# Kernel tuning notes

Hardware: AMD Instinct MI355X
Metric: run time of the kernel (lower is better)

The kernel has to match this reference:

```python
import jax, jax.numpy as jnp
import numpy as np

L = 2       # num_layers
D = 256     # d_model
DFF = 1024  # d_ffn
NH = 8      # n_heads
NP = 4      # n_points
CIN = 512   # in_channels
B = 8
HH = 64
WW = 64
EPS = 1e-5


def setup_inputs() -> dict:
    key = jax.random.key(0)
    ks = iter(jax.random.split(key, 48))
    def w(shape, s=0.02):
        return jax.random.normal(next(ks), shape, jnp.float32) * s
    inp = dict(
        x=jax.random.normal(next(ks), (B, CIN, HH, WW), jnp.float32),
        W_in=w((D, CIN)),
        bn1_g=jnp.ones((D,), jnp.float32), bn1_b=jnp.zeros((D,), jnp.float32),
        bn1_m=jnp.zeros((D,), jnp.float32), bn1_v=jnp.ones((D,), jnp.float32),
        query_embed=w((HH * WW, D), 1.0),
        Woff=w((L, D, NH * NP * 2)), boff=w((L, NH * NP * 2), 2.0),
        Wattn=w((L, D, NH * NP)), battn=jnp.zeros((L, NH * NP), jnp.float32),
        Wval=w((L, D, D)), bval=jnp.zeros((L, D), jnp.float32),
        Wo=w((L, D, D)), bo=jnp.zeros((L, D), jnp.float32),
        ln1_g=jnp.ones((L, D), jnp.float32), ln1_b=jnp.zeros((L, D), jnp.float32),
        W1=w((L, D, DFF)), b1=jnp.zeros((L, DFF), jnp.float32),
        W2=w((L, DFF, D)), b2=jnp.zeros((L, D), jnp.float32),
        ln2_g=jnp.ones((L, D), jnp.float32), ln2_b=jnp.zeros((L, D), jnp.float32),
        W_out=w((CIN, D)),
        bn2_g=jnp.ones((CIN,), jnp.float32), bn2_b=jnp.zeros((CIN,), jnp.float32),
        bn2_m=jnp.zeros((CIN,), jnp.float32), bn2_v=jnp.ones((CIN,), jnp.float32),
    )
    return inp


def layer_norm(x, g, b):
    m = jnp.mean(x, axis=-1, keepdims=True)
    v = jnp.mean((x - m) ** 2, axis=-1, keepdims=True)
    return (x - m) * jax.lax.rsqrt(v + EPS) * g + b


def bilinear_sample(value, loc, Hh, Ww):
    # value: (B, NH, dh, H*W); loc: (B, Lq, NH, NP, 2) normalized to [0,1]
    # Matches F.grid_sample(align_corners=False, padding_mode='zeros') with grid=2*loc-1.
    Bn, Lq, nH, P, _ = loc.shape
    gx = loc[..., 0] * Ww - 0.5
    gy = loc[..., 1] * Hh - 0.5
    x0 = jnp.floor(gx)
    y0 = jnp.floor(gy)
    wx = gx - x0
    wy = gy - y0
    x0i = x0.astype(jnp.int32)
    y0i = y0.astype(jnp.int32)

    def t(a):  # (B,Lq,NH,P) -> (B,NH,1,Lq*P)
        return jnp.transpose(a, (0, 2, 1, 3)).reshape(Bn, nH, 1, Lq * P)

    def gather(xi, yi):
        valid = (xi >= 0) & (xi < Ww) & (yi >= 0) & (yi < Hh)
        xc = jnp.clip(xi, 0, Ww - 1)
        yc = jnp.clip(yi, 0, Hh - 1)
        idx = t(yc * Ww + xc)  # (B,NH,1,Lq*P)
        v = jnp.take_along_axis(value, idx, axis=3)  # (B,NH,dh,Lq*P)
        return v * t(valid).astype(value.dtype)

    v00 = gather(x0i, y0i)
    v10 = gather(x0i + 1, y0i)
    v01 = gather(x0i, y0i + 1)
    v11 = gather(x0i + 1, y0i + 1)
    wxt = t(wx)
    wyt = t(wy)
    out = (v00 * (1 - wxt) * (1 - wyt) + v10 * wxt * (1 - wyt)
           + v01 * (1 - wxt) * wyt + v11 * wxt * wyt)
    return out.reshape(Bn, nH, -1, Lq, P)  # (B,NH,dh,Lq,NP)


def reference(x, W_in, bn1_g, bn1_b, bn1_m, bn1_v, query_embed,
              Woff, boff, Wattn, battn, Wval, bval, Wo, bo,
              ln1_g, ln1_b, W1, b1, W2, b2, ln2_g, ln2_b,
              W_out, bn2_g, bn2_b, bn2_m, bn2_v):
    Bn, C, Hh, Ww = x.shape
    HW = Hh * Ww
    dh = D // NH

    # proj_in: 1x1 conv (no bias) + BN (inference) + ReLU
    xp = jnp.einsum('bchw,dc->bdhw', x, W_in)
    xp = (xp - bn1_m[:, None, None]) * jax.lax.rsqrt(bn1_v[:, None, None] + EPS)
    xp = jax.nn.relu(xp * bn1_g[:, None, None] + bn1_b[:, None, None])
    src = xp.reshape(Bn, D, HW).transpose(0, 2, 1)  # (B, HW, D)

    # reference points: centers of pixels, normalized
    ry = (jnp.arange(Hh, dtype=jnp.float32) + 0.5) / Hh
    rx = (jnp.arange(Ww, dtype=jnp.float32) + 0.5) / Ww
    yy, xx = jnp.meshgrid(ry, rx, indexing='ij')
    refpts = jnp.stack([xx, yy], axis=-1).reshape(HW, 2)  # (HW, 2) as (x, y)
    norm = jnp.array([Ww, Hh], jnp.float32)

    q = jnp.broadcast_to(query_embed[None], (Bn, HW, D))
    for i in range(L):
        # --- MSDeformAttn (n_levels=1) ---
        val = (src @ Wval[i] + bval[i]).reshape(Bn, HW, NH, dh)
        val = val.transpose(0, 2, 3, 1)  # (B, NH, dh, HW)
        off = (q @ Woff[i] + boff[i]).reshape(Bn, HW, NH, NP, 2)
        attn = jax.nn.softmax((q @ Wattn[i] + battn[i]).reshape(Bn, HW, NH, NP), axis=-1)
        loc = refpts[None, :, None, None, :] + off / norm  # (B, HW, NH, NP, 2)
        samp = bilinear_sample(val, loc, Hh, Ww)  # (B, NH, dh, HW, NP)
        o = jnp.einsum('bhdqp,bhqp->bqhd', samp, attn.transpose(0, 2, 1, 3))
        o = o.reshape(Bn, HW, D) @ Wo[i] + bo[i]
        q = layer_norm(q + o, ln1_g[i], ln1_b[i])
        # --- FFN ---
        ffn = jax.nn.relu(q @ W1[i] + b1[i]) @ W2[i] + b2[i]
        q = layer_norm(q + ffn, ln2_g[i], ln2_b[i])

    # proj_out: 1x1 conv (no bias) + BN (inference) + ReLU
    y = q.transpose(0, 2, 1).reshape(Bn, D, Hh, Ww)
    y = jnp.einsum('bdhw,cd->bchw', y, W_out)
    y = (y - bn2_m[:, None, None]) * jax.lax.rsqrt(bn2_v[:, None, None] + EPS)
    return jax.nn.relu(y * bn2_g[:, None, None] + bn2_b[:, None, None])
```

## Files before the change

### kernel.cpp

```cpp
#include <hip/hip_runtime.h>
#include <cstdint>

#define LYR 2
#define DM  256
#define DFFN 1024
#define CINC 512
#define BBATCH 8
#define HWTOT 4096
#define EPSV 1e-5f

using u16 = unsigned short;
typedef __attribute__((ext_vector_type(8))) short bf16x8;
typedef __attribute__((ext_vector_type(4))) float f32x4;

__device__ inline u16 f2b(float v) {
    union { float f; uint32_t u; } x; x.f = v;
    uint32_t r = x.u + 0x7fffu + ((x.u >> 16) & 1u);
    return (u16)(r >> 16);
}
__device__ inline uint32_t pk2(float a, float b) {
    return (uint32_t)f2b(a) | ((uint32_t)f2b(b) << 16);
}
__device__ inline float blo(uint32_t d) {
    union { uint32_t i; float f; } x; x.i = d << 16; return x.f;
}
__device__ inline float bhi(uint32_t d) {
    union { uint32_t i; float f; } x; x.i = d & 0xffff0000u; return x.f;
}

template<int MODE>
__global__ __launch_bounds__(256) void mfma_gemm(
    const u16* __restrict__ A, const u16* __restrict__ Bt,
    const float* __restrict__ scale, const float* __restrict__ shift,
    void* __restrict__ Cv, int M, int N, int K, int ldc,
    long long a_zs, long long b_zs, long long c_zs, int swz, int gxlog)
{
    __shared__ u16 As[4][4096];
    __shared__ u16 Bs[4][4096];
    const int tid = threadIdx.x;
    const int lane = tid & 63;
    const int wid = tid >> 6;
    const int wm = (wid & 1) << 6, wn = (wid >> 1) << 6;
    const int quad = lane >> 4, r = lane & 15;

    int bx = blockIdx.x, by = blockIdx.y;
    if (swz) {
        int linear = by * gridDim.x + bx;
        int xcd = linear & 7;
        int s = linear >> 3;
        bx = s & (gridDim.x - 1);
        by = xcd * (gridDim.y >> 3) + (s >> gxlog);
    }
    const int m0 = by << 7, n0 = bx << 7;
    const u16* Ab = A + (long long)blockIdx.z * a_zs + (long long)m0 * K;
    const u16* Bb = Bt + (long long)blockIdx.z * b_zs + (long long)n0 * K;

    const int u0 = tid, u1 = tid + 256;
    const int mu0 = u0 >> 2, cu0 = (u0 & 3) ^ ((mu0 >> 1) & 3);
    const int mu1 = u1 >> 2, cu1 = (u1 & 3) ^ ((mu1 >> 1) & 3);
    const long long ga0 = (long long)mu0 * K + cu0 * 8;
    const long long ga1 = (long long)mu1 * K + cu1 * 8;

    int aoff[4], boff[4];
#pragma unroll
    for (int t = 0; t < 4; ++t) {
        int m = wm + t * 16 + r;
        aoff[t] = (m * 4 + (quad ^ ((m >> 1) & 3))) * 8;
        int n = wn + t * 16 + r;
        boff[t] = (n * 4 + (quad ^ ((n >> 1) & 3))) * 8;
    }

    f32x4 acc[4][4];
#pragma unroll
    for (int i = 0; i < 4; ++i)
#pragma unroll
        for (int j = 0; j < 4; ++j) acc[i][j] = (f32x4){0.f, 0.f, 0.f, 0.f};

    const int NT = K >> 5;

#define GSTAGE(g, b) do {                                                                       \
    const long long kk = (long long)(g) << 5;                                                   \
    __builtin_amdgcn_global_load_lds((const __attribute__((address_space(1))) void*)(Ab + ga0 + kk), \
        (__attribute__((address_space(3))) void*)(&As[b][u0 * 8]), 16, 0, 0);                   \
    __builtin_amdgcn_global_load_lds((const __attribute__((address_space(1))) void*)(Ab + ga1 + kk), \
        (__attribute__((address_space(3))) void*)(&As[b][u1 * 8]), 16, 0, 0);                   \
    __builtin_amdgcn_global_load_lds((const __attribute__((address_space(1))) void*)(Bb + ga0 + kk), \
        (__attribute__((address_space(3))) void*)(&Bs[b][u0 * 8]), 16, 0, 0);                   \
    __builtin_amdgcn_global_load_lds((const __attribute__((address_space(1))) void*)(Bb + ga1 + kk), \
        (__attribute__((address_space(3))) void*)(&Bs[b][u1 * 8]), 16, 0, 0);                   \
} while (0)

    GSTAGE(0, 0);
    GSTAGE(1, 1);
    GSTAGE(2, 2);

    for (int t = 0; t < NT; ++t) {
        if (t < NT - 2)       asm volatile("s_waitcnt vmcnt(8)" ::: "memory");
        else if (t == NT - 2) asm volatile("s_waitcnt vmcnt(4)" ::: "memory");
        else                  asm volatile("s_waitcnt vmcnt(0)" ::: "memory");
        __builtin_amdgcn_s_barrier();
        __builtin_amdgcn_sched_barrier(0);
        if (t + 3 < NT) GSTAGE(t + 3, (t + 3) & 3);
        const u16* Ap = As[t & 3];
        const u16* Bp = Bs[t & 3];
        bf16x8 af[4], bf[4];
#pragma unroll
        for (int tt = 0; tt < 4; ++tt) af[tt] = *(const bf16x8*)(Ap + aoff[tt]);
#pragma unroll
        for (int tt = 0; tt < 4; ++tt) bf[tt] = *(const bf16x8*)(Bp + boff[tt]);
#pragma unroll
        for (int i = 0; i < 4; ++i)
#pragma unroll
            for (int j = 0; j < 4; ++j)
                acc[i][j] = __builtin_amdgcn_mfma_f32_16x16x32_bf16(bf[j], af[i], acc[i][j], 0, 0, 0);
    }
#undef GSTAGE

    const long long zc = (long long)blockIdx.z * c_zs;
    float4 sh4[4], sc4[4];
    if (MODE != 3) {
#pragma unroll
        for (int j = 0; j < 4; ++j) {
            int colb = n0 + wn + j * 16 + quad * 4;
            sh4[j] = *(const float4*)&shift[colb];
            if (MODE == 1) sc4[j] = *(const float4*)&scale[colb];
        }
    }
#pragma unroll
    for (int i = 0; i < 4; ++i) {
        const int row = m0 + wm + i * 16 + r;
        float rsc = 0.f, rsh = 0.f;
        if (MODE == 3) { rsc = scale[row]; rsh = shift[row]; }
#pragma unroll
        for (int j = 0; j < 4; ++j) {
            const int colb = n0 + wn + j * 16 + quad * 4;
            f32x4 v = acc[i][j];
            if (MODE == 0) {
                uint2 o;
                o.x = pk2(v[0] + sh4[j].x, v[1] + sh4[j].y);
                o.y = pk2(v[2] + sh4[j].z, v[3] + sh4[j].w);
                *(uint2*)((u16*)Cv + zc + (long long)row * ldc + colb) = o;
            } else if (MODE == 1) {
                uint2 o;
                o.x = pk2(fmaxf(v[0] * sc4[j].x + sh4[j].x, 0.f), fmaxf(v[1] * sc4[j].y + sh4[j].y, 0.f));
                o.y = pk2(fmaxf(v[2] * sc4[j].z + sh4[j].z, 0.f), fmaxf(v[3] * sc4[j].w + sh4[j].w, 0.f));
                *(uint2*)((u16*)Cv + zc + (long long)row * ldc + colb) = o;
            } else if (MODE == 2) {
                float4 o = {v[0] + sh4[j].x, v[1] + sh4[j].y, v[2] + sh4[j].z, v[3] + sh4[j].w};
                *(float4*)((float*)Cv + zc + (long long)row * ldc + colb) = o;
            } else {
                float4 o = {fmaxf(v[0] * rsc + rsh, 0.f), fmaxf(v[1] * rsc + rsh, 0.f),
                            fmaxf(v[2] * rsc + rsh, 0.f), fmaxf(v[3] * rsc + rsh, 0.f)};
                *(float4*)((float*)Cv + zc + (long long)row * ldc + colb) = o;
            }
        }
    }
}

__global__ __launch_bounds__(512, 4) void mfma_gemm_ln(
    const u16* __restrict__ A, const u16* __restrict__ Bf,
    const float* __restrict__ bias,
    float* __restrict__ q, u16* __restrict__ q16,
    const float* __restrict__ g, const float* __restrict__ beta, int K)
{
    __shared__ u16 As[3][2048];
    __shared__ float red_s[8][64], red_ss[8][64];
    const int tid = threadIdx.x;
    const int lane = tid & 63;
    const int w = tid >> 6;
    const int quad = lane >> 4, r = lane & 15;
    const int m0 = blockIdx.x << 6;
    const u16* Ab = A + (long long)m0 * K;

    const int mA = tid >> 2, cA = (tid & 3) ^ ((mA >> 1) & 3);
    const long long gaA = (long long)mA * K + cA * 8;
    const bool stager = tid < 256;

    int aoff[4];
#pragma unroll
    for (int t = 0; t < 4; ++t) {
        int m = t * 16 + r;
        aoff[t] = (m * 4 + (quad ^ ((m >> 1) & 3))) * 8;
    }

    const u16* Bw = Bf + ((size_t)(2 * w) * 64 + lane) * 8;

    f32x4 acc[4][2];
#pragma unroll
    for (int i = 0; i < 4; ++i)
#pragma unroll
        for (int j = 0; j < 2; ++j) acc[i][j] = (f32x4){0.f, 0.f, 0.f, 0.f};

    const int NT = K >> 5;

    if (stager) {
        __builtin_amdgcn_global_load_lds((const __attribute__((address_space(1))) void*)(Ab + gaA),
                                         (__attribute__((address_space(3))) void*)(&As[0][tid * 8]), 16, 0, 0);
        __builtin_amdgcn_global_load_lds((const __attribute__((address_space(1))) void*)(Ab + gaA + 32),
                                         (__attribute__((address_space(3))) void*)(&As[1][tid * 8]), 16, 0, 0);
    }
    __builtin_amdgcn_sched_barrier(0);
    bf16x8 bc0 = *(const bf16x8*)(Bw);
    bf16x8 bc1 = *(const bf16x8*)(Bw + 512);

    int cb = 0;
    for (int t = 0; t < NT; ++t) {
        asm volatile("s_waitcnt vmcnt(3)" ::: "memory");
        __builtin_amdgcn_s_barrier();
        __builtin_amdgcn_sched_barrier(0);
        int nb = cb + 2; if (nb >= 3) nb -= 3;
        if (stager && t + 2 < NT)
            __builtin_amdgcn_global_load_lds((const __attribute__((address_space(1))) void*)(Ab + gaA + (long long)(t + 2) * 32),
                                             (__attribute__((address_space(3))) void*)(&As[nb][tid * 8]), 16, 0, 0);
        bf16x8 bn0, bn1;
        if (t + 1 < NT) {
            const u16* Bn = Bw + (size_t)(t + 1) * 8192;
            bn0 = *(const bf16x8*)(Bn);
            bn1 = *(const bf16x8*)(Bn + 512);
        } else { bn0 = bc0; bn1 = bc1; }

        const u16* Ac = As[cb];
        bf16x8 af[4];
#pragma unroll
        for (int tt = 0; tt < 4; ++tt) af[tt] = *(const bf16x8*)(Ac + aoff[tt]);
#pragma unroll
        for (int i = 0; i < 4; ++i) {
            acc[i][0] = __builtin_amdgcn_mfma_f32_16x16x32_bf16(bc0, af[i], acc[i][0], 0, 0, 0);
            acc[i][1] = __builtin_amdgcn_mfma_f32_16x16x32_bf16(bc1, af[i], acc[i][1], 0, 0, 0);
        }
        bc0 = bn0; bc1 = bn1;
        cb = (cb + 1 == 3) ? 0 : cb + 1;
    }

    float4 sh2[2];
#pragma unroll
    for (int j = 0; j < 2; ++j)
        sh2[j] = *(const float4*)&bias[w * 32 + j * 16 + quad * 4];

    float s_[4] = {0.f, 0.f, 0.f, 0.f}, ss_[4] = {0.f, 0.f, 0.f, 0.f};
#pragma unroll
    for (int i = 0; i < 4; ++i) {
        const int row = m0 + i * 16 + r;
#pragma unroll
        for (int j = 0; j < 2; ++j) {
            const int colb = w * 32 + j * 16 + quad * 4;
            float4 qo = *(const float4*)&q[(size_t)row * DM + colb];
            acc[i][j][0] += sh2[j].x + qo.x;
            acc[i][j][1] += sh2[j].y + qo.y;
            acc[i][j][2] += sh2[j].z + qo.z;
            acc[i][j][3] += sh2[j].w + qo.w;
#pragma unroll
            for (int e = 0; e < 4; ++e) {
                s_[i] += acc[i][j][e];
                ss_[i] += acc[i][j][e] * acc[i][j][e];
            }
        }
    }
#pragma unroll
    for (int i = 0; i < 4; ++i) {
        s_[i] += __shfl_xor(s_[i], 16);  ss_[i] += __shfl_xor(ss_[i], 16);
        s_[i] += __shfl_xor(s_[i], 32);  ss_[i] += __shfl_xor(ss_[i], 32);
    }
    if (quad == 0) {
#pragma unroll
        for (int i = 0; i < 4; ++i) {
            red_s[w][i * 16 + r] = s_[i];
            red_ss[w][i * 16 + r] = ss_[i];
        }
    }
    __syncthreads();

    float mean[4], rstd[4];
#pragma unroll
    for (int i = 0; i < 4; ++i) {
        float S = 0.f, SS = 0.f;
#pragma unroll
        for (int w2 = 0; w2 < 8; ++w2) { S += red_s[w2][i * 16 + r]; SS += red_ss[w2][i * 16 + r]; }
        mean[i] = S * (1.0f / 256.0f);
        rstd[i] = rsqrtf(SS * (1.0f / 256.0f) - mean[i] * mean[i] + EPSV);
    }

    float4 g4[2], bt4[2];
#pragma unroll
    for (int j = 0; j < 2; ++j) {
        int colb = w * 32 + j * 16 + quad * 4;
        g4[j] = *(const float4*)&g[colb];
        bt4[j] = *(const float4*)&beta[colb];
    }
#pragma unroll
    for (int i = 0; i < 4; ++i) {
        const int row = m0 + i * 16 + r;
#pragma unroll
        for (int j = 0; j < 2; ++j) {
            const int colb = w * 32 + j * 16 + quad * 4;
            float o0 = (acc[i][j][0] - mean[i]) * rstd[i] * g4[j].x + bt4[j].x;
            float o1 = (acc[i][j][1] - mean[i]) * rstd[i] * g4[j].y + bt4[j].y;
            float o2 = (acc[i][j][2] - mean[i]) * rstd[i] * g4[j].z + bt4[j].z;
            float o3 = (acc[i][j][3] - mean[i]) * rstd[i] * g4[j].w + bt4[j].w;
            *(float4*)&q[(size_t)row * DM + colb] = make_float4(o0, o1, o2, o3);
            *(uint2*)(q16 + (size_t)row * DM + colb) = make_uint2(pk2(o0, o1), pk2(o2, o3));
        }
    }
}

__global__ __launch_bounds__(512) void ffn_fused(
    const u16* __restrict__ q16in, const u16* __restrict__ w1F, const u16* __restrict__ w2F,
    const float* __restrict__ b1, const float* __restrict__ b2,
    float* __restrict__ q, u16* __restrict__ q16,
    const float* __restrict__ g, const float* __restrict__ beta)
{
    __shared__ u16 Aq[16384];
    __shared__ u16 hF[16384];
    __shared__ float red_s[8][64], red_ss[8][64];
    const int tid = threadIdx.x;
    const int lane = tid & 63;
    const int w = tid >> 6;
    const int quad = lane >> 4, r = lane & 15;
    const int m0 = blockIdx.x << 6;

    const u16* Ab = q16in + (long long)m0 * DM;
#pragma unroll
    for (int i = 0; i < 4; ++i) {
        int u = tid + i * 512;
        int ks = u >> 8, v = u & 255;
        int m = v >> 2, c = (v & 3) ^ ((m >> 1) & 3);
        __builtin_amdgcn_global_load_lds((const __attribute__((address_space(1))) void*)(Ab + (long long)m * DM + ks * 32 + c * 8),
                                         (__attribute__((address_space(3))) void*)(Aq + u * 8), 16, 0, 0);
    }

    int aoff[4];
#pragma unroll
    for (int t = 0; t < 4; ++t) {
        int m = t * 16 + r;
        aoff[t] = (m * 4 + (quad ^ ((m >> 1) & 3))) * 8;
    }

    f32x4 acc2[4][2];
#pragma unroll
    for (int i = 0; i < 4; ++i)
#pragma unroll
        for (int j = 0; j < 2; ++j) acc2[i][j] = (f32x4){0.f, 0.f, 0.f, 0.f};

    __syncthreads();

    for (int qq = 0; qq < 4; ++qq) {
        f32x4 acc1[4][2];
#pragma unroll
        for (int i = 0; i < 4; ++i)
#pragma unroll
            for (int j = 0; j < 2; ++j) acc1[i][j] = (f32x4){0.f, 0.f, 0.f, 0.f};
        __builtin_amdgcn_s_setprio(1);
#pragma unroll
        for (int ks = 0; ks < 8; ++ks) {
            const u16* bp = w1F + ((size_t)(ks * 64 + qq * 16 + w * 2) * 64 + lane) * 8;
            bf16x8 bf0 = *(const bf16x8*)bp;
            bf16x8 bf1 = *(const bf16x8*)(bp + 512);
            bf16x8 af[4];
#pragma unroll
            for (int t = 0; t < 4; ++t) af[t] = *(const bf16x8*)(Aq + ks * 2048 + aoff[t]);
#pragma unroll
            for (int i = 0; i < 4; ++i) {
                acc1[i][0] = __builtin_amdgcn_mfma_f32_16x16x32_bf16(bf0, af[i], acc1[i][0], 0, 0, 0);
                acc1[i][1] = __builtin_amdgcn_mfma_f32_16x16x32_bf16(bf1, af[i], acc1[i][1], 0, 0, 0);
            }
        }
        __builtin_amdgcn_s_setprio(0);
        __syncthreads();

#pragma unroll
        for (int j = 0; j < 2; ++j) {
            const int cb = qq * 256 + w * 32 + j * 16 + quad * 4;
            const float4 b14 = *(const float4*)&b1[cb];
            const int lane2 = r | (((j * 2 + (quad >> 1)) & 3) << 4);
            const int eo = (quad & 1) * 4;
#pragma unroll
            for (int i = 0; i < 4; ++i) {
                f32x4 v = acc1[i][j];
                uint2 o;
                o.x = pk2(fmaxf(v[0] + b14.x, 0.f), fmaxf(v[1] + b14.y, 0.f));
                o.y = pk2(fmaxf(v[2] + b14.z, 0.f), fmaxf(v[3] + b14.w, 0.f));
                *(uint2*)(hF + ((w * 4 + i) * 64 + lane2) * 8 + eo) = o;
            }
        }
        __syncthreads();

        __builtin_amdgcn_s_setprio(1);
#pragma unroll
        for (int ks = 0; ks < 8; ++ks) {
            const u16* bp = w2F + ((size_t)((qq * 8 + ks) * 16 + w * 2) * 64 + lane) * 8;
            bf16x8 bf0 = *(const bf16x8*)bp;
            bf16x8 bf1 = *(const bf16x8*)(bp + 512);
            bf16x8 af[4];
#pragma unroll
            for (int t = 0; t < 4; ++t) af[t] = *(const bf16x8*)(hF + ((ks * 4 + t) * 64 + lane) * 8);
#pragma unroll
            for (int i = 0; i < 4; ++i) {
                acc2[i][0] = __builtin_amdgcn_mfma_f32_16x16x32_bf16(bf0, af[i], acc2[i][0], 0, 0, 0);
                acc2[i][1] = __builtin_amdgcn_mfma_f32_16x16x32_bf16(bf1, af[i], acc2[i][1], 0, 0, 0);
            }
        }
        __builtin_amdgcn_s_setprio(0);
    }

    float4 sh2[2];
#pragma unroll
    for (int j = 0; j < 2; ++j)
        sh2[j] = *(const float4*)&b2[w * 32 + j * 16 + quad * 4];

    float s_[4] = {0.f, 0.f, 0.f, 0.f}, ss_[4] = {0.f, 0.f, 0.f, 0.f};
#pragma unroll
    for (int i = 0; i < 4; ++i) {
        const int row = m0 + i * 16 + r;
#pragma unroll
        for (int j = 0; j < 2; ++j) {
            const int colb = w * 32 + j * 16 + quad * 4;
            float4 qo = *(const float4*)&q[(size_t)row * DM + colb];
            acc2[i][j][0] += sh2[j].x + qo.x;
            acc2[i][j][1] += sh2[j].y + qo.y;
            acc2[i][j][2] += sh2[j].z + qo.z;
            acc2[i][j][3] += sh2[j].w + qo.w;
#pragma unroll
            for (int e = 0; e < 4; ++e) {
                s_[i] += acc2[i][j][e];
                ss_[i] += acc2[i][j][e] * acc2[i][j][e];
            }
        }
    }
#pragma unroll
    for (int i = 0; i < 4; ++i) {
        s_[i] += __shfl_xor(s_[i], 16);  ss_[i] += __shfl_xor(ss_[i], 16);
        s_[i] += __shfl_xor(s_[i], 32);  ss_[i] += __shfl_xor(ss_[i], 32);
    }
    if (quad == 0) {
#pragma unroll
        for (int i = 0; i < 4; ++i) {
            red_s[w][i * 16 + r] = s_[i];
            red_ss[w][i * 16 + r] = ss_[i];
        }
    }
    __syncthreads();

    float mean[4], rstd[4];
#pragma unroll
    for (int i = 0; i < 4; ++i) {
        float S = 0.f, SS = 0.f;
#pragma unroll
        for (int w2 = 0; w2 < 8; ++w2) { S += red_s[w2][i * 16 + r]; SS += red_ss[w2][i * 16 + r]; }
        mean[i] = S * (1.0f / 256.0f);
        rstd[i] = rsqrtf(SS * (1.0f / 256.0f) - mean[i] * mean[i] + EPSV);
    }

    float4 g4[2], bt4[2];
#pragma unroll
    for (int j = 0; j < 2; ++j) {
        int colb = w * 32 + j * 16 + quad * 4;
        g4[j] = *(const float4*)&g[colb];
        bt4[j] = *(const float4*)&beta[colb];
    }
#pragma unroll
    for (int i = 0; i < 4; ++i) {
        const int row = m0 + i * 16 + r;
#pragma unroll
        for (int j = 0; j < 2; ++j) {
            const int colb = w * 32 + j * 16 + quad * 4;
            float o0 = (acc2[i][j][0] - mean[i]) * rstd[i] * g4[j].x + bt4[j].x;
            float o1 = (acc2[i][j][1] - mean[i]) * rstd[i] * g4[j].y + bt4[j].y;
            float o2 = (acc2[i][j][2] - mean[i]) * rstd[i] * g4[j].z + bt4[j].z;
            float o3 = (acc2[i][j][3] - mean[i]) * rstd[i] * g4[j].w + bt4[j].w;
            *(float4*)&q[(size_t)row * DM + colb] = make_float4(o0, o1, o2, o3);
            *(uint2*)(q16 + (size_t)row * DM + colb) = make_uint2(pk2(o0, o1), pk2(o2, o3));
        }
    }
}

__device__ __attribute__((noinline)) void tconv(const float* src, u16* dst, int K, int N, int tk, int tn)
{
    __shared__ float t[32][33];
    const int tx = threadIdx.x & 31, ty = threadIdx.x >> 5;
#pragma unroll
    for (int i = 0; i < 4; ++i)
        t[ty + i * 8][tx] = src[(size_t)(tk * 32 + ty + i * 8) * N + tn * 32 + tx];
    __syncthreads();
#pragma unroll
    for (int i = 0; i < 4; ++i)
        dst[(size_t)(tn * 32 + ty + i * 8) * K + tk * 32 + tx] = f2b(t[tx][ty + i * 8]);
}

__device__ __attribute__((noinline)) void tconv_oa(const float* Woff, const float* Wattn, u16* dst, int tk, int tn)
{
    __shared__ float t[32][33];
    const int tx = threadIdx.x & 31, ty = threadIdx.x >> 5;
#pragma unroll
    for (int i = 0; i < 4; ++i) {
        int k = tk * 32 + ty + i * 8, n = tn * 32 + tx;
        float v = (n < 64) ? Woff[k * 64 + n] : ((n < 96) ? Wattn[k * 32 + n - 64] : 0.f);
        t[ty + i * 8][tx] = v;
    }
    __syncthreads();
#pragma unroll
    for (int i = 0; i < 4; ++i)
        dst[(size_t)(tn * 32 + ty + i * 8) * 256 + tk * 32 + tx] = f2b(t[tx][ty + i * 8]);
}

__device__ __attribute__((noinline)) void frag_prep(const float* W, u16* dst, int ks, int nc, int N)
{
    __shared__ float t[32][256];
    const int tid = threadIdx.x;
#pragma unroll
    for (int kk = 0; kk < 32; ++kk)
        t[kk][tid] = W[(size_t)(ks * 32 + kk) * N + nc * 256 + tid];
    __syncthreads();
    const int NT16 = N >> 4;
#pragma unroll
    for (int i = 0; i < 4; ++i) {
        int idx = tid + i * 256;
        int nt = idx >> 6, l = idx & 63;
        int n = nt * 16 + (l & 15);
        int kb = (l >> 4) * 8;
        u16 o[8];
#pragma unroll
        for (int e = 0; e < 8; ++e) o[e] = f2b(t[kb + e][n]);
        *(uint4*)(dst + ((size_t)(ks * NT16 + nc * 16 + nt) * 64 + l) * 8) = *(const uint4*)o;
    }
}

__global__ __launch_bounds__(256) void prep_weights(
    const float* __restrict__ Wval, const float* __restrict__ Wo,
    const float* __restrict__ W1, const float* __restrict__ W2,
    const float* __restrict__ Woff, const float* __restrict__ Wattn,
    const float* __restrict__ boff, const float* __restrict__ battn,
    const float* __restrict__ W_in, const float* __restrict__ W_out,
    const float* __restrict__ bn1g, const float* __restrict__ bn1b,
    const float* __restrict__ bn1m, const float* __restrict__ bn1v,
    const float* __restrict__ bn2g, const float* __restrict__ bn2b,
    const float* __restrict__ bn2m, const float* __restrict__ bn2v,
    u16* __restrict__ wvalT, u16* __restrict__ woF, u16* __restrict__ w1F,
    u16* __restrict__ w2F, u16* __restrict__ woaT,
    u16* __restrict__ winC, u16* __restrict__ woutC,
    float* __restrict__ bn1sc, float* __restrict__ bn1sh,
    float* __restrict__ bn2sc, float* __restrict__ bn2sh, float* __restrict__ boa)
{
    int bid = blockIdx.x;
    if (bid < 128) {
        int l = bid >> 6, r2 = bid & 63;
        tconv(Wval + l * 65536, wvalT + l * 65536, 256, 256, r2 & 7, r2 >> 3);
    } else if (bid < 192) {
        int i2 = bid - 128, l = i2 >> 5, r2 = i2 & 31;
        tconv_oa(Woff + l * 16384, Wattn + l * 8192, woaT + l * 32768, r2 & 7, r2 >> 3);
    } else if (bid < 208) {
        int i2 = bid - 192;
        frag_prep(Wo + (i2 >> 3) * 65536, woF + (i2 >> 3) * 65536, i2 & 7, 0, 256);
    } else if (bid < 272) {
        int i2 = bid - 208, l = i2 >> 5, r2 = i2 & 31;
        frag_prep(W1 + l * 262144, w1F + l * 262144, r2 >> 2, r2 & 3, 1024);
    } else if (bid < 336) {
        int i2 = bid - 272;
        frag_prep(W2 + (i2 >> 5) * 262144, w2F + (i2 >> 5) * 262144, i2 & 31, 0, 256);
    } else if (bid < 368) {
        int g2 = bid - 336, base = g2 * 4096, t = threadIdx.x;
#pragma unroll
        for (int k = 0; k < 16; ++k) winC[base + k * 256 + t] = f2b(W_in[base + k * 256 + t]);
    } else if (bid < 400) {
        int g2 = bid - 368, base = g2 * 4096, t = threadIdx.x;
#pragma unroll
        for (int k = 0; k < 16; ++k) woutC[base + k * 256 + t] = f2b(W_out[base + k * 256 + t]);
    } else {
        int t = threadIdx.x;
        { float s = bn1g[t] * rsqrtf(bn1v[t] + EPSV); bn1sc[t] = s; bn1sh[t] = bn1b[t] - bn1m[t] * s; }
        for (int c = 0; c < 2; ++c) {
            int i = c * 256 + t;
            float s = bn2g[i] * rsqrtf(bn2v[i] + EPSV);
            bn2sc[i] = s; bn2sh[i] = bn2b[i] - bn2m[i] * s;
        }
        if (t < 128)
            for (int l = 0; l < 2; ++l)
                boa[l * 128 + t] = (t < 64) ? boff[l * 64 + t]
                                 : ((t < 96) ? battn[l * 32 + t - 64] : 0.f);
    }
}

__global__ __launch_bounds__(256) void transpose_x(const float* __restrict__ x, u16* __restrict__ xT)
{
    __shared__ float t[64][65];
    const int b = blockIdx.z, p0 = blockIdx.y << 6, c0 = blockIdx.x << 6;
    const int tx = threadIdx.x & 63, ty = threadIdx.x >> 6;
    const float* xb = x + ((size_t)b * CINC + c0) * HWTOT + p0;
#pragma unroll
    for (int i = 0; i < 16; ++i)
        t[ty + i * 4][tx] = xb[(size_t)(ty + i * 4) * HWTOT + tx];
    __syncthreads();
    u16* xo = xT + ((size_t)b * HWTOT + p0) * CINC + c0;
#pragma unroll
    for (int i = 0; i < 16; ++i)
        xo[(size_t)(ty + i * 4) * CINC + tx] = f2b(t[tx][ty + i * 4]);
}

struct IW { int eo; float w; };

__global__ __launch_bounds__(256) void sample_kernel(
    const u16* __restrict__ val,
    const float* __restrict__ oa,
    u16* __restrict__ oms)
{
    __shared__ float s_oa[8][96];
    __shared__ IW s_iw[8][32][5];
    const int t = threadIdx.x;
    const int bq0 = blockIdx.x << 3;
    const int b = blockIdx.x >> 9;

    {
        int qi = t >> 5, j = t & 31;
        if (j < 24)
            ((float4*)s_oa[qi])[j] = ((const float4*)oa)[((size_t)(bq0 + qi)) * 32 + j];
    }
    __syncthreads();

    {
        const int qi = t >> 5, hp = t & 31, h = hp >> 2, p = hp & 3;
        const float* so = s_oa[qi];
        float l0 = so[64 + h * 4 + 0], l1 = so[64 + h * 4 + 1];
        float l2 = so[64 + h * 4 + 2], l3 = so[64 + h * 4 + 3];
        float mx = fmaxf(fmaxf(l0, l1), fmaxf(l2, l3));
        float e0 = __expf(l0 - mx), e1 = __expf(l1 - mx), e2 = __expf(l2 - mx), e3 = __expf(l3 - mx);
        float inv = 1.0f / (e0 + e1 + e2 + e3);
        float aw = ((p == 0) ? e0 : (p == 1) ? e1 : (p == 2) ? e2 : e3) * inv;
        const int bq = bq0 + qi;
        float gx = (float)(bq & 63) + so[hp * 2 + 0];
        float gy = (float)((bq >> 6) & 63) + so[hp * 2 + 1];
        float x0f = floorf(gx), y0f = floorf(gy);
        float wx = gx - x0f, wy = gy - y0f;
        int x0 = (int)x0f, y0 = (int)y0f;
#pragma unroll
        for (int c = 0; c < 4; ++c) {
            int xi = x0 + (c & 1), yi = y0 + (c >> 1);
            bool ok = (xi >= 0) && (xi < 64) && (yi >= 0) && (yi < 64);
            float wgt = ((c & 1) ? wx : 1.0f - wx) * ((c >> 1) ? wy : 1.0f - wy);
            s_iw[qi][hp][c].eo = ok ? ((yi * 64 + xi) << 8) : 0;
            s_iw[qi][hp][c].w = ok ? aw * wgt : 0.f;
        }
    }
    __syncthreads();

    {
        const int qi = t >> 5, l = t & 31, h = l >> 2, cc = l & 3;
        const u16* base = val + ((size_t)b << 20) + (h << 5) + (cc << 3);
        float a[8] = {0.f, 0.f, 0.f, 0.f, 0.f, 0.f, 0.f, 0.f};
#pragma unroll
        for (int p = 0; p < 4; ++p)
#pragma unroll
            for (int c = 0; c < 4; ++c) {
                IW iw = s_iw[qi][(h << 2) + p][c];
                uint4 v = *(const uint4*)(base + iw.eo);
                a[0] += iw.w * blo(v.x); a[1] += iw.w * bhi(v.x);
                a[2] += iw.w * blo(v.y); a[3] += iw.w * bhi(v.y);
                a[4] += iw.w * blo(v.z); a[5] += iw.w * bhi(v.z);
                a[6] += iw.w * blo(v.w); a[7] += iw.w * bhi(v.w);
            }
        uint4 o;
        o.x = (uint32_t)f2b(a[0]) | ((uint32_t)f2b(a[1]) << 16);
        o.y = (uint32_t)f2b(a[2]) | ((uint32_t)f2b(a[3]) << 16);
        o.z = (uint32_t)f2b(a[4]) | ((uint32_t)f2b(a[5]) << 16);
        o.w = (uint32_t)f2b(a[6]) | ((uint32_t)f2b(a[7]) << 16);
        *(uint4*)(oms + (size_t)(bq0 + qi) * 256 + (h << 5) + (cc << 3)) = o;
    }
}

__global__ __launch_bounds__(256) void bcast_q(
    const float4* __restrict__ qe, float4* __restrict__ q, u16* __restrict__ q16)
{
    const int i = blockIdx.x * 256 + threadIdx.x;
    float4 v = qe[i];
    uint2 pk = make_uint2(pk2(v.x, v.y), pk2(v.z, v.w));
#pragma unroll
    for (int b = 0; b < BBATCH; ++b) {
        q[(size_t)b * 262144 + i] = v;
        ((uint2*)q16)[(size_t)b * 262144 + i] = pk;
    }
}

extern "C" void kernel_launch(void* const* d_in, const int* in_sizes, int n_in,
                              void* d_out, int out_size, void* d_ws, size_t ws_size,
                              hipStream_t stream)
{
    (void)in_sizes; (void)n_in; (void)out_size; (void)ws_size;
    const float* x     = (const float*)d_in[0];
    const float* W_in  = (const float*)d_in[1];
    const float* bn1_g = (const float*)d_in[2];
    const float* bn1_b = (const float*)d_in[3];
    const float* bn1_m = (const float*)d_in[4];
    const float* bn1_v = (const float*)d_in[5];
    const float* qe    = (const float*)d_in[6];
    const float* Woff  = (const float*)d_in[7];
    const float* boff  = (const float*)d_in[8];
    const float* Wattn = (const float*)d_in[9];
    const float* battn = (const float*)d_in[10];
    const float* Wval  = (const float*)d_in[11];
    const float* bval  = (const float*)d_in[12];
    const float* Wo    = (const float*)d_in[13];
    const float* bo    = (const float*)d_in[14];
    const float* ln1_g = (const float*)d_in[15];
    const float* ln1_b = (const float*)d_in[16];
    const float* W1    = (const float*)d_in[17];
    const float* b1    = (const float*)d_in[18];
    const float* W2    = (const float*)d_in[19];
    const float* b2    = (const float*)d_in[20];
    const float* ln2_g = (const float*)d_in[21];
    const float* ln2_b = (const float*)d_in[22];
    const float* W_out = (const float*)d_in[23];
    const float* bn2_g = (const float*)d_in[24];
    const float* bn2_b = (const float*)d_in[25];
    const float* bn2_m = (const float*)d_in[26];
    const float* bn2_v = (const float*)d_in[27];
    float* out = (float*)d_out;

    char* w = (char*)d_ws;
    char* pool    = w;          w += 67108864;
    float* q      = (float*)w;  w += 33554432;
    u16*  q16     = (u16*)w;    w += 16777216;
    u16*  src16   = (u16*)w;    w += 16777216;
    u16*  wvalT   = (u16*)w;    w += 262144;
    u16*  woF     = (u16*)w;    w += 262144;
    u16*  w1F     = (u16*)w;    w += 1048576;
    u16*  w2F     = (u16*)w;    w += 1048576;
    u16*  woaT    = (u16*)w;    w += 131072;
    u16*  winC    = (u16*)w;    w += 262144;
    u16*  woutC   = (u16*)w;    w += 262144;
    float* bn1sc  = (float*)w;  w += 1024;
    float* bn1sh  = (float*)w;  w += 1024;
    float* bn2sc  = (float*)w;  w += 2048;
    float* bn2sh  = (float*)w;  w += 2048;
    float* boa    = (float*)w;  w += 1024;

    u16*  xT     = (u16*)pool;
    u16*  val16  = (u16*)pool;
    float* offat = (float*)(pool + 16777216);
    u16*  oms16  = (u16*)(pool + 33554432);

    prep_weights<<<dim3(401), 256, 0, stream>>>(
        Wval, Wo, W1, W2, Woff, Wattn, boff, battn, W_in, W_out,
        bn1_g, bn1_b, bn1_m, bn1_v, bn2_g, bn2_b, bn2_m, bn2_v,
        wvalT, woF, w1F, w2F, woaT, winC, woutC, bn1sc, bn1sh, bn2sc, bn2sh, boa);
    transpose_x<<<dim3(CINC / 64, HWTOT / 64, BBATCH), 256, 0, stream>>>(x, xT);
    bcast_q<<<dim3(1024), 256, 0, stream>>>((const float4*)qe, (float4*)q, q16);

    mfma_gemm<1><<<dim3(2, 256, 1), 256, 0, stream>>>(
        xT, winC, bn1sc, bn1sh, src16, 32768, 256, 512, 256, 0, 0, 0, 1, 1);

    for (int l = 0; l < LYR; ++l) {
        mfma_gemm<0><<<dim3(2, 256, 1), 256, 0, stream>>>(
            src16, wvalT + l * 65536, nullptr, bval + l * 256, val16,
            32768, 256, 256, 256, 0, 0, 0, 1, 1);
        mfma_gemm<2><<<dim3(1, 256, 1), 256, 0, stream>>>(
            q16, woaT + l * 32768, nullptr, boa + l * 128, offat,
            32768, 128, 256, 128, 0, 0, 0, 1, 0);
        sample_kernel<<<dim3(4096), 256, 0, stream>>>(val16, offat, oms16);
        mfma_gemm_ln<<<dim3(512), 512, 0, stream>>>(
            oms16, woF + l * 65536, bo + l * 256, q, q16,
            ln1_g + l * 256, ln1_b + l * 256, 256);
        ffn_fused<<<dim3(512), 512, 0, stream>>>(
            q16, w1F + l * 262144, w2F + l * 262144,
            b1 + l * 1024, b2 + l * 256, q, q16,
            ln2_g + l * 256, ln2_b + l * 256);
    }

    mfma_gemm<3><<<dim3(32, 4, BBATCH), 256, 0, stream>>>(
        woutC, q16, bn2sc, bn2sh, out, 512, 4096, 256, 4096,
        0, (long long)HWTOT * DM, (long long)CINC * HWTOT, 0, 0);
}
```

Baseline: 458.1 us.

## Fuse deformable sampling into output-projection LayerNorm GEMM; shrink FFN hidden chunk

Bilinear sampling with the attention softmax moves into the Wo-projection+LayerNorm kernel. Each thread samples one query/head into a 32-channel register accumulator and writes the bf16 result straight into swizzled shared memory as the GEMM A operand, so the intermediate sampled tensor no longer makes a global round trip. The FFN kernel now processes 128-wide hidden chunks instead of 256, halving the hidden LDS buffer and hinting 6 waves per SIMD via launch bounds, with lighter barriers. The fused kernel has fewer threads doing the gather (512 per 64 queries), so its latency hiding may suffer, and the register pressure from 32 accumulators is high.

```diff
diff --git a/kernel.cpp b/kernel.cpp
--- a/kernel.cpp
+++ b/kernel.cpp
@@ -157,79 +157,109 @@
     }
 }
 
-__global__ __launch_bounds__(512, 4) void mfma_gemm_ln(
-    const u16* __restrict__ A, const u16* __restrict__ Bf,
+__global__ __launch_bounds__(512) void attn_out_ln(
+    const u16* __restrict__ val,
+    const float* __restrict__ oa,
+    const u16* __restrict__ Bf,
     const float* __restrict__ bias,
     float* __restrict__ q, u16* __restrict__ q16,
-    const float* __restrict__ g, const float* __restrict__ beta, int K)
-{
-    __shared__ u16 As[3][2048];
+    const float* __restrict__ g, const float* __restrict__ beta)
+{
+    __shared__ u16 Aq[16384];
     __shared__ float red_s[8][64], red_ss[8][64];
     const int tid = threadIdx.x;
     const int lane = tid & 63;
     const int w = tid >> 6;
     const int quad = lane >> 4, r = lane & 15;
     const int m0 = blockIdx.x << 6;
-    const u16* Ab = A + (long long)m0 * K;
-
-    const int mA = tid >> 2, cA = (tid & 3) ^ ((mA >> 1) & 3);
-    const long long gaA = (long long)mA * K + cA * 8;
-    const bool stager = tid < 256;
-
-    int aoff[4];
+
+    {
+        const int qi = tid >> 3, h = tid & 7;
+        const int bq = m0 + qi;
+        const int b = m0 >> 12;
+        const float* row = oa + (size_t)bq * 128;
+        float4 o01 = *(const float4*)(row + h * 8);
+        float4 o23 = *(const float4*)(row + h * 8 + 4);
+        float4 lg  = *(const float4*)(row + 64 + h * 4);
+        float mx = fmaxf(fmaxf(lg.x, lg.y), fmaxf(lg.z, lg.w));
+        float e0 = __expf(lg.x - mx), e1 = __expf(lg.y - mx);
+        float e2 = __expf(lg.z - mx), e3 = __expf(lg.w - mx);
+        float inv = 1.0f / (e0 + e1 + e2 + e3);
+        const float aw[4] = {e0 * inv, e1 * inv, e2 * inv, e3 * inv};
+        const float offx[4] = {o01.x, o01.z, o23.x, o23.z};
+        const float offy[4] = {o01.y, o01.w, o23.y, o23.w};
+        const float fx = (float)(bq & 63), fy = (float)((bq >> 6) & 63);
+        const u16* vb = val + ((size_t)b << 20) + h * 32;
+        float a[32];
+#pragma unroll
+        for (int d = 0; d < 32; ++d) a[d] = 0.f;
+#pragma unroll
+        for (int p = 0; p < 4; ++p) {
+            float gx = fx + offx[p], gy = fy + offy[p];
+            float x0f = floorf(gx), y0f = floorf(gy);
+            float wx = gx - x0f, wy = gy - y0f;
+            int x0 = (int)x0f, y0 = (int)y0f;
+#pragma unroll
+            for (int c = 0; c < 4; ++c) {
+                int xi = x0 + (c & 1), yi = y0 + (c >> 1);
+                bool ok = (xi >= 0) && (xi < 64) && (yi >= 0) && (yi < 64);
+                float wgt = ((c & 1) ? wx : 1.0f - wx) * ((c >> 1) ? wy : 1.0f - wy);
+                wgt = ok ? aw[p] * wgt : 0.f;
+                int eo = ok ? ((yi * 64 + xi) << 8) : 0;
+                const uint4* s4 = (const uint4*)(vb + eo);
+#pragma unroll
+                for (int d4 = 0; d4 < 4; ++d4) {
+                    uint4 v = s4[d4];
+                    a[d4 * 8 + 0] += wgt * blo(v.x); a[d4 * 8 + 1] += wgt * bhi(v.x);
+                    a[d4 * 8 + 2] += wgt * blo(v.y); a[d4 * 8 + 3] += wgt * bhi(v.y);
+                    a[d4 * 8 + 4] += wgt * blo(v.z); a[d4 * 8 + 5] += wgt * bhi(v.z);
+                    a[d4 * 8 + 6] += wgt * blo(v.w); a[d4 * 8 + 7] += wgt * bhi(v.w);
+                }
+            }
+        }
+        const int sw = (qi >> 1) & 3;
+        const int hx = (h & 3) << 3;
+        u16* dst = Aq + h * 2048;
+#pragma unroll
+        for (int qd = 0; qd < 4; ++qd) {
+            uint4 o4;
+            o4.x = pk2(a[qd * 8 + 0], a[qd * 8 + 1]);
+            o4.y = pk2(a[qd * 8 + 2], a[qd * 8 + 3]);
+            o4.z = pk2(a[qd * 8 + 4], a[qd * 8 + 5]);
+            o4.w = pk2(a[qd * 8 + 6], a[qd * 8 + 7]);
+            *(uint4*)(dst + (((qi * 4 + (qd ^ sw)) * 8) ^ hx)) = o4;
+        }
+    }
+    __syncthreads();
+
+    int aoff0[4];
 #pragma unroll
     for (int t = 0; t < 4; ++t) {
         int m = t * 16 + r;
-        aoff[t] = (m * 4 + (quad ^ ((m >> 1) & 3))) * 8;
-    }
-
+        aoff0[t] = (m * 4 + (quad ^ ((m >> 1) & 3))) * 8;
+    }
     const u16* Bw = Bf + ((size_t)(2 * w) * 64 + lane) * 8;
-
     f32x4 acc[4][2];
 #pragma unroll
     for (int i = 0; i < 4; ++i)
 #pragma unroll
         for (int j = 0; j < 2; ++j) acc[i][j] = (f32x4){0.f, 0.f, 0.f, 0.f};
 
-    const int NT = K >> 5;
-
-    if (stager) {
-        __builtin_amdgcn_global_load_lds((const __attribute__((address_space(1))) void*)(Ab + gaA),
-                                         (__attribute__((address_space(3))) void*)(&As[0][tid * 8]), 16, 0, 0);
-        __builtin_amdgcn_global_load_lds((const __attribute__((address_space(1))) void*)(Ab + gaA + 32),
-                                         (__attribute__((address_space(3))) void*)(&As[1][tid * 8]), 16, 0, 0);
-    }
-    __builtin_amdgcn_sched_barrier(0);
-    bf16x8 bc0 = *(const bf16x8*)(Bw);
-    bf16x8 bc1 = *(const bf16x8*)(Bw + 512);
-
-    int cb = 0;
-    for (int t = 0; t < NT; ++t) {
-        asm volatile("s_waitcnt vmcnt(3)" ::: "memory");
-        __builtin_amdgcn_s_barrier();
-        __builtin_amdgcn_sched_barrier(0);
-        int nb = cb + 2; if (nb >= 3) nb -= 3;
-        if (stager && t + 2 < NT)
-            __builtin_amdgcn_global_load_lds((const __attribute__((address_space(1))) void*)(Ab + gaA + (long long)(t + 2) * 32),
-                                             (__attribute__((address_space(3))) void*)(&As[nb][tid * 8]), 16, 0, 0);
-        bf16x8 bn0, bn1;
-        if (t + 1 < NT) {
-            const u16* Bn = Bw + (size_t)(t + 1) * 8192;
-            bn0 = *(const bf16x8*)(Bn);
-            bn1 = *(const bf16x8*)(Bn + 512);
-        } else { bn0 = bc0; bn1 = bc1; }
-
-        const u16* Ac = As[cb];
+#pragma unroll
+    for (int ks = 0; ks < 8; ++ks) {
+        const u16* bp = Bw + (size_t)ks * 8192;
+        bf16x8 bf0 = *(const bf16x8*)bp;
+        bf16x8 bf1 = *(const bf16x8*)(bp + 512);
+        const int kx = (ks & 3) << 3;
         bf16x8 af[4];
 #pragma unroll
-        for (int tt = 0; tt < 4; ++tt) af[tt] = *(const bf16x8*)(Ac + aoff[tt]);
+        for (int t = 0; t < 4; ++t)
+            af[t] = *(const bf16x8*)(Aq + ks * 2048 + (aoff0[t] ^ kx));
 #pragma unroll
         for (int i = 0; i < 4; ++i) {
-            acc[i][0] = __builtin_amdgcn_mfma_f32_16x16x32_bf16(bc0, af[i], acc[i][0], 0, 0, 0);
-            acc[i][1] = __builtin_amdgcn_mfma_f32_16x16x32_bf16(bc1, af[i], acc[i][1], 0, 0, 0);
-        }
-        bc0 = bn0; bc1 = bn1;
-        cb = (cb + 1 == 3) ? 0 : cb + 1;
+            acc[i][0] = __builtin_amdgcn_mfma_f32_16x16x32_bf16(bf0, af[i], acc[i][0], 0, 0, 0);
+            acc[i][1] = __builtin_amdgcn_mfma_f32_16x16x32_bf16(bf1, af[i], acc[i][1], 0, 0, 0);
+        }
     }
 
     float4 sh2[2];
@@ -303,14 +333,14 @@
     }
 }
 
-__global__ __launch_bounds__(512) void ffn_fused(
+__global__ __launch_bounds__(512, 6) void ffn_fused(
     const u16* __restrict__ q16in, const u16* __restrict__ w1F, const u16* __restrict__ w2F,
     const float* __restrict__ b1, const float* __restrict__ b2,
     float* __restrict__ q, u16* __restrict__ q16,
     const float* __restrict__ g, const float* __restrict__ beta)
 {
     __shared__ u16 Aq[16384];
-    __shared__ u16 hF[16384];
+    __shared__ u16 hF[8192];
     __shared__ float red_s[8][64], red_ss[8][64];
     const int tid = threadIdx.x;
     const int lane = tid & 63;
@@ -335,6 +365,9 @@
         aoff[t] = (m * 4 + (quad ^ ((m >> 1) & 3))) * 8;
     }
 
+    const int X = 4 * w + quad;
+    const int packbase = (X >> 3) * 2048 + ((X & 7) >> 1) * 128 + r * 8 + (X & 1) * 4;
+
     f32x4 acc2[4][2];
 #pragma unroll
     for (int i = 0; i < 4; ++i)
@@ -343,51 +376,46 @@
 
     __syncthreads();
 
-    for (int qq = 0; qq < 4; ++qq) {
-        f32x4 acc1[4][2];
-#pragma unroll
-        for (int i = 0; i < 4; ++i)
-#pragma unroll
-            for (int j = 0; j < 2; ++j) acc1[i][j] = (f32x4){0.f, 0.f, 0.f, 0.f};
+    for (int cch = 0; cch < 8; ++cch) {
+        f32x4 acc1[4];
+#pragma unroll
+        for (int i = 0; i < 4; ++i) acc1[i] = (f32x4){0.f, 0.f, 0.f, 0.f};
         __builtin_amdgcn_s_setprio(1);
 #pragma unroll
         for (int ks = 0; ks < 8; ++ks) {
-            const u16* bp = w1F + ((size_t)(ks * 64 + qq * 16 + w * 2) * 64 + lane) * 8;
-            bf16x8 bf0 = *(const bf16x8*)bp;
-            bf16x8 bf1 = *(const bf16x8*)(bp + 512);
+            const u16* bp = w1F + ((size_t)(ks * 64 + cch * 8 + w) * 64 + lane) * 8;
+            bf16x8 bf = *(const bf16x8*)bp;
             bf16x8 af[4];
 #pragma unroll
             for (int t = 0; t < 4; ++t) af[t] = *(const bf16x8*)(Aq + ks * 2048 + aoff[t]);
 #pragma unroll
+            for (int i = 0; i < 4; ++i)
+                acc1[i] = __builtin_amdgcn_mfma_f32_16x16x32_bf16(bf, af[i], acc1[i], 0, 0, 0);
+        }
+        __builtin_amdgcn_s_setprio(0);
+        __builtin_amdgcn_sched_barrier(0);
+        __builtin_amdgcn_s_barrier();
+
+        {
+            const int cb = cch * 128 + w * 16 + quad * 4;
+            const float4 b14 = *(const float4*)&b1[cb];
+#pragma unroll
             for (int i = 0; i < 4; ++i) {
-                acc1[i][0] = __builtin_amdgcn_mfma_f32_16x16x32_bf16(bf0, af[i], acc1[i][0], 0, 0, 0);
-                acc1[i][1] = __builtin_amdgcn_mfma_f32_16x16x32_bf16(bf1, af[i], acc1[i][1], 0, 0, 0);
-            }
-        }
-        __builtin_amdgcn_s_setprio(0);
-        __syncthreads();
-
-#pragma unroll
-        for (int j = 0; j < 2; ++j) {
-            const int cb = qq * 256 + w * 32 + j * 16 + quad * 4;
-            const float4 b14 = *(const float4*)&b1[cb];
-            const int lane2 = r | (((j * 2 + (quad >> 1)) & 3) << 4);
-            const int eo = (quad & 1) * 4;
-#pragma unroll
-            for (int i = 0; i < 4; ++i) {
-                f32x4 v = acc1[i][j];
+                f32x4 v = acc1[i];
                 uint2 o;
                 o.x = pk2(fmaxf(v[0] + b14.x, 0.f), fmaxf(v[1] + b14.y, 0.f));
                 o.y = pk2(fmaxf(v[2] + b14.z, 0.f), fmaxf(v[3] + b14.w, 0.f));
-                *(uint2*)(hF + ((w * 4 + i) * 64 + lane2) * 8 + eo) = o;
+                *(uint2*)(hF + packbase + i * 512) = o;
             }
         }
-        __syncthreads();
+        asm volatile("s_waitcnt lgkmcnt(0)" ::: "memory");
+        __builtin_amdgcn_s_barrier();
+        __builtin_amdgcn_sched_barrier(0);
 
         __builtin_amdgcn_s_setprio(1);
 #pragma unroll
-        for (int ks = 0; ks < 8; ++ks) {
-            const u16* bp = w2F + ((size_t)((qq * 8 + ks) * 16 + w * 2) * 64 + lane) * 8;
+        for (int ks = 0; ks < 4; ++ks) {
+            const u16* bp = w2F + ((size_t)((cch * 4 + ks) * 16 + w * 2) * 64 + lane) * 8;
             bf16x8 bf0 = *(const bf16x8*)bp;
             bf16x8 bf1 = *(const bf16x8*)(bp + 512);
             bf16x8 af[4];
@@ -593,76 +621,6 @@
 #pragma unroll
     for (int i = 0; i < 16; ++i)
         xo[(size_t)(ty + i * 4) * CINC + tx] = f2b(t[tx][ty + i * 4]);
-}
-
-struct IW { int eo; float w; };
-
-__global__ __launch_bounds__(256) void sample_kernel(
-    const u16* __restrict__ val,
-    const float* __restrict__ oa,
-    u16* __restrict__ oms)
-{
-    __shared__ float s_oa[8][96];
-    __shared__ IW s_iw[8][32][5];
-    const int t = threadIdx.x;
-    const int bq0 = blockIdx.x << 3;
-    const int b = blockIdx.x >> 9;
-
-    {
-        int qi = t >> 5, j = t & 31;
-        if (j < 24)
-            ((float4*)s_oa[qi])[j] = ((const float4*)oa)[((size_t)(bq0 + qi)) * 32 + j];
-    }
-    __syncthreads();
-
-    {
-        const int qi = t >> 5, hp = t & 31, h = hp >> 2, p = hp & 3;
-        const float* so = s_oa[qi];
-        float l0 = so[64 + h * 4 + 0], l1 = so[64 + h * 4 + 1];
-        float l2 = so[64 + h * 4 + 2], l3 = so[64 + h * 4 + 3];
-        float mx = fmaxf(fmaxf(l0, l1), fmaxf(l2, l3));
-        float e0 = __expf(l0 - mx), e1 = __expf(l1 - mx), e2 = __expf(l2 - mx), e3 = __expf(l3 - mx);
-        float inv = 1.0f / (e0 + e1 + e2 + e3);
-        float aw = ((p == 0) ? e0 : (p == 1) ? e1 : (p == 2) ? e2 : e3) * inv;
-        const int bq = bq0 + qi;
-        float gx = (float)(bq & 63) + so[hp * 2 + 0];
-        float gy = (float)((bq >> 6) & 63) + so[hp * 2 + 1];
-        float x0f = floorf(gx), y0f = floorf(gy);
-        float wx = gx - x0f, wy = gy - y0f;
-        int x0 = (int)x0f, y0 = (int)y0f;
-#pragma unroll
-        for (int c = 0; c < 4; ++c) {
-            int xi = x0 + (c & 1), yi = y0 + (c >> 1);
-            bool ok = (xi >= 0) && (xi < 64) && (yi >= 0) && (yi < 64);
-            float wgt = ((c & 1) ? wx : 1.0f - wx) * ((c >> 1) ? wy : 1.0f - wy);
-            s_iw[qi][hp][c].eo = ok ? ((yi * 64 + xi) << 8) : 0;
-            s_iw[qi][hp][c].w = ok ? aw * wgt : 0.f;
-        }
-    }
-    __syncthreads();
-
-    {
-        const int qi = t >> 5, l = t & 31, h = l >> 2, cc = l & 3;
-        const u16* base = val + ((size_t)b << 20) + (h << 5) + (cc << 3);
-        float a[8] = {0.f, 0.f, 0.f, 0.f, 0.f, 0.f, 0.f, 0.f};
-#pragma unroll
-        for (int p = 0; p < 4; ++p)
-#pragma unroll
-            for (int c = 0; c < 4; ++c) {
-                IW iw = s_iw[qi][(h << 2) + p][c];
-                uint4 v = *(const uint4*)(base + iw.eo);
-                a[0] += iw.w * blo(v.x); a[1] += iw.w * bhi(v.x);
-                a[2] += iw.w * blo(v.y); a[3] += iw.w * bhi(v.y);
-                a[4] += iw.w * blo(v.z); a[5] += iw.w * bhi(v.z);
-                a[6] += iw.w * blo(v.w); a[7] += iw.w * bhi(v.w);
-            }
-        uint4 o;
-        o.x = (uint32_t)f2b(a[0]) | ((uint32_t)f2b(a[1]) << 16);
-        o.y = (uint32_t)f2b(a[2]) | ((uint32_t)f2b(a[3]) << 16);
-        o.z = (uint32_t)f2b(a[4]) | ((uint32_t)f2b(a[5]) << 16);
-        o.w = (uint32_t)f2b(a[6]) | ((uint32_t)f2b(a[7]) << 16);
-        *(uint4*)(oms + (size_t)(bq0 + qi) * 256 + (h << 5) + (cc << 3)) = o;
-    }
 }
 
 __global__ __launch_bounds__(256) void bcast_q(
@@ -734,7 +692,6 @@
     u16*  xT     = (u16*)pool;
     u16*  val16  = (u16*)pool;
     float* offat = (float*)(pool + 16777216);
-    u16*  oms16  = (u16*)(pool + 33554432);
 
     prep_weights<<<dim3(401), 256, 0, stream>>>(
         Wval, Wo, W1, W2, Woff, Wattn, boff, battn, W_in, W_out,
@@ -753,10 +710,9 @@
         mfma_gemm<2><<<dim3(1, 256, 1), 256, 0, stream>>>(
             q16, woaT + l * 32768, nullptr, boa + l * 128, offat,
             32768, 128, 256, 128, 0, 0, 0, 1, 0);
-        sample_kernel<<<dim3(4096), 256, 0, stream>>>(val16, offat, oms16);
-        mfma_gemm_ln<<<dim3(512), 512, 0, stream>>>(
-            oms16, woF + l * 65536, bo + l * 256, q, q16,
-            ln1_g + l * 256, ln1_b + l * 256, 256);
+        attn_out_ln<<<dim3(512), 512, 0, stream>>>(
+            val16, offat, woF + l * 65536, bo + l * 256, q, q16,
+            ln1_g + l * 256, ln1_b + l * 256);
         ffn_fused<<<dim3(512), 512, 0, stream>>>(
             q16, w1F + l * 262144, w2F + l * 262144,
             b1 + l * 1024, b2 + l * 256, q, q16,
```

After: 574.2 us. +25.4%, slower.

## Halve FFN hidden chunk width to shrink LDS and accumulators in ffn_fused

Applied to the files above, without the earlier changes.

The fused FFN kernel now processes the 1024-wide hidden dimension in 8 chunks of 128 instead of 4 chunks of 256. This halves the intermediate LDS buffer and the first-GEMM accumulator registers, and a launch-bounds hint asks for more resident waves. The hidden-activation packing layout is recomputed to match, and explicit s_barrier with sched_barrier replaces __syncthreads. In exchange there are twice as many chunk iterations and barriers, and each W1 load feeds fewer MFMAs.

```diff
diff --git a/kernel.cpp b/kernel.cpp
--- a/kernel.cpp
+++ b/kernel.cpp
@@ -303,14 +303,14 @@
     }
 }
 
-__global__ __launch_bounds__(512) void ffn_fused(
+__global__ __launch_bounds__(512, 6) void ffn_fused(
     const u16* __restrict__ q16in, const u16* __restrict__ w1F, const u16* __restrict__ w2F,
     const float* __restrict__ b1, const float* __restrict__ b2,
     float* __restrict__ q, u16* __restrict__ q16,
     const float* __restrict__ g, const float* __restrict__ beta)
 {
     __shared__ u16 Aq[16384];
-    __shared__ u16 hF[16384];
+    __shared__ u16 hF[8192];
     __shared__ float red_s[8][64], red_ss[8][64];
     const int tid = threadIdx.x;
     const int lane = tid & 63;
@@ -335,6 +335,9 @@
         aoff[t] = (m * 4 + (quad ^ ((m >> 1) & 3))) * 8;
     }
 
+    const int X = 4 * w + quad;
+    const int packbase = (X >> 3) * 2048 + ((X & 7) >> 1) * 128 + r * 8 + (X & 1) * 4;
+
     f32x4 acc2[4][2];
 #pragma unroll
     for (int i = 0; i < 4; ++i)
@@ -343,51 +346,46 @@
 
     __syncthreads();
 
-    for (int qq = 0; qq < 4; ++qq) {
-        f32x4 acc1[4][2];
-#pragma unroll
-        for (int i = 0; i < 4; ++i)
-#pragma unroll
-            for (int j = 0; j < 2; ++j) acc1[i][j] = (f32x4){0.f, 0.f, 0.f, 0.f};
+    for (int cch = 0; cch < 8; ++cch) {
+        f32x4 acc1[4];
+#pragma unroll
+        for (int i = 0; i < 4; ++i) acc1[i] = (f32x4){0.f, 0.f, 0.f, 0.f};
         __builtin_amdgcn_s_setprio(1);
 #pragma unroll
         for (int ks = 0; ks < 8; ++ks) {
-            const u16* bp = w1F + ((size_t)(ks * 64 + qq * 16 + w * 2) * 64 + lane) * 8;
-            bf16x8 bf0 = *(const bf16x8*)bp;
-            bf16x8 bf1 = *(const bf16x8*)(bp + 512);
+            const u16* bp = w1F + ((size_t)(ks * 64 + cch * 8 + w) * 64 + lane) * 8;
+            bf16x8 bf = *(const bf16x8*)bp;
             bf16x8 af[4];
 #pragma unroll
             for (int t = 0; t < 4; ++t) af[t] = *(const bf16x8*)(Aq + ks * 2048 + aoff[t]);
 #pragma unroll
+            for (int i = 0; i < 4; ++i)
+                acc1[i] = __builtin_amdgcn_mfma_f32_16x16x32_bf16(bf, af[i], acc1[i], 0, 0, 0);
+        }
+        __builtin_amdgcn_s_setprio(0);
+        __builtin_amdgcn_sched_barrier(0);
+        __builtin_amdgcn_s_barrier();
+
+        {
+            const int cb = cch * 128 + w * 16 + quad * 4;
+            const float4 b14 = *(const float4*)&b1[cb];
+#pragma unroll
             for (int i = 0; i < 4; ++i) {
-                acc1[i][0] = __builtin_amdgcn_mfma_f32_16x16x32_bf16(bf0, af[i], acc1[i][0], 0, 0, 0);
-                acc1[i][1] = __builtin_amdgcn_mfma_f32_16x16x32_bf16(bf1, af[i], acc1[i][1], 0, 0, 0);
-            }
-        }
-        __builtin_amdgcn_s_setprio(0);
-        __syncthreads();
-
-#pragma unroll
-        for (int j = 0; j < 2; ++j) {
-            const int cb = qq * 256 + w * 32 + j * 16 + quad * 4;
-            const float4 b14 = *(const float4*)&b1[cb];
-            const int lane2 = r | (((j * 2 + (quad >> 1)) & 3) << 4);
-            const int eo = (quad & 1) * 4;
-#pragma unroll
-            for (int i = 0; i < 4; ++i) {
-                f32x4 v = acc1[i][j];
+                f32x4 v = acc1[i];
                 uint2 o;
                 o.x = pk2(fmaxf(v[0] + b14.x, 0.f), fmaxf(v[1] + b14.y, 0.f));
                 o.y = pk2(fmaxf(v[2] + b14.z, 0.f), fmaxf(v[3] + b14.w, 0.f));
-                *(uint2*)(hF + ((w * 4 + i) * 64 + lane2) * 8 + eo) = o;
+                *(uint2*)(hF + packbase + i * 512) = o;
             }
         }
-        __syncthreads();
+        asm volatile("s_waitcnt lgkmcnt(0)" ::: "memory");
+        __builtin_amdgcn_s_barrier();
+        __builtin_amdgcn_sched_barrier(0);
 
         __builtin_amdgcn_s_setprio(1);
 #pragma unroll
-        for (int ks = 0; ks < 8; ++ks) {
-            const u16* bp = w2F + ((size_t)((qq * 8 + ks) * 16 + w * 2) * 64 + lane) * 8;
+        for (int ks = 0; ks < 4; ++ks) {
+            const u16* bp = w2F + ((size_t)((cch * 4 + ks) * 16 + w * 2) * 64 + lane) * 8;
             bf16x8 bf0 = *(const bf16x8*)bp;
             bf16x8 bf1 = *(const bf16x8*)(bp + 512);
             bf16x8 af[4];
```

Measured after the change: 504.8 us. +10.2%, slower.
